# Kernel tuning notes

Hardware: AMD Instinct MI355X
Metric: run time of the kernel (lower is better)

## Reference

```python
import jax, jax.numpy as jnp
import numpy as np

P, N, H, W, K = 100000, 8, 256, 256, 8
EPS = 1e-12  # F.normalize clamp_min eps


def setup_inputs() -> dict:
    key = jax.random.key(0)
    ks = jax.random.split(key, 12)
    normals = jax.random.normal(ks[3], (P, 3), jnp.float32)
    normals = normals / jnp.linalg.norm(normals, axis=-1, keepdims=True)
    return {
        "idx": jax.random.randint(ks[0], (N, H, W, K), 0, P),
        "dists": jax.random.uniform(ks[1], (N, H, W, K), dtype=jnp.float32),
        "points": jax.random.normal(ks[2], (P, 3), jnp.float32),
        "normals": normals,
        "light_location": jax.random.normal(ks[4], (1, 3), jnp.float32) * 2.0,
        "light_ambient": jax.random.uniform(ks[5], (1, 3), dtype=jnp.float32),
        "light_diffuse": jax.random.uniform(ks[6], (1, 3), dtype=jnp.float32),
        "light_specular": jax.random.uniform(ks[7], (1, 3), dtype=jnp.float32),
        "mat_ambient": jax.random.uniform(ks[8], (1, 3), dtype=jnp.float32),
        "mat_diffuse": jax.random.uniform(ks[9], (1, 3), dtype=jnp.float32),
        "mat_specular": jax.random.uniform(ks[10], (1, 3), dtype=jnp.float32),
        "camera_position": jax.random.normal(ks[11], (1, 3), jnp.float32) * 3.0,
        "shininess": 64,
    }


def _normalize(v):
    return v / jnp.clip(jnp.linalg.norm(v, axis=-1, keepdims=True), 1e-6)


def reference(idx, dists, points, normals, light_location, light_ambient,
              light_diffuse, light_specular, mat_ambient, mat_diffuse,
              mat_specular, camera_position, shininess):
    # masked gather: invalid (idx < 0) pixels read point 0
    safe_idx = jnp.where(idx < 0, 0, idx)                      # (N,H,W,K)
    pix_pts = points[safe_idx]                                 # (N,H,W,K,3)
    pix_nrm = normals[safe_idx]                                # (N,H,W,K,3)

    # point-light Phong shading (pytorch3d _apply_lighting)
    dir_light = _normalize(light_location - pix_pts)           # (N,H,W,K,3)
    cos = jnp.sum(pix_nrm * dir_light, axis=-1, keepdims=True)  # (N,H,W,K,1)
    diffuse = light_diffuse * jax.nn.relu(cos) * mat_diffuse

    view = _normalize(camera_position - pix_pts)
    reflect = 2.0 * cos * pix_nrm - dir_light
    alpha = jax.nn.relu(jnp.sum(view * reflect, axis=-1)) * (cos[..., 0] > 0)
    specular = light_specular * (alpha ** shininess)[..., None] * mat_specular

    ambient = light_ambient * mat_ambient                      # (1,3) broadcast
    colors = ambient + diffuse + specular                      # (N,H,W,K,3)

    # L1-normalized distance weights over K, weighted sum
    dist_mask = jnp.where(dists != -1.0, dists, 0.0)
    wn = dist_mask / jnp.clip(jnp.sum(jnp.abs(dist_mask), axis=-1, keepdims=True), EPS)
    images = jnp.sum(wn[..., None] * colors, axis=-2)          # (N,H,W,3)
    return images
```

## Files before the change

### kernel.cpp

```cpp
#include <hip/hip_runtime.h>

#define K 8

typedef float vfloat4 __attribute__((ext_vector_type(4)));
typedef int   vint4   __attribute__((ext_vector_type(4)));

__global__ __launch_bounds__(256) void pack_pn_kernel(
    const float* __restrict__ points,
    const float* __restrict__ normals,
    vfloat4*     __restrict__ rec,
    int P)
{
    const int i = blockIdx.x * blockDim.x + threadIdx.x;
    if (i >= P) return;
    const size_t b = (size_t)i * 3;
    vfloat4 pv = {points[b],  points[b + 1],  points[b + 2],  0.0f};
    vfloat4 nv = {normals[b], normals[b + 1], normals[b + 2], 0.0f};
    rec[2 * i]     = pv;
    rec[2 * i + 1] = nv;
}

template <bool PACKED>
__global__ __launch_bounds__(256) void shading_compositor_kernel(
    const int*    __restrict__ idx,
    const float*  __restrict__ dists,
    const float*  __restrict__ points,
    const float*  __restrict__ normals,
    const vfloat4* __restrict__ rec,
    const float*  __restrict__ light_location,
    const float*  __restrict__ light_ambient,
    const float*  __restrict__ light_diffuse,
    const float*  __restrict__ light_specular,
    const float*  __restrict__ mat_ambient,
    const float*  __restrict__ mat_diffuse,
    const float*  __restrict__ mat_specular,
    const float*  __restrict__ camera_position,
    const int*    __restrict__ shininess_p,
    float*        __restrict__ out,
    int n_pix)
{
    const int p = blockIdx.x * blockDim.x + threadIdx.x;
    if (p >= n_pix) return;

    const vint4*   idxv = reinterpret_cast<const vint4*>(idx   + (size_t)p * K);
    const vfloat4* dstv = reinterpret_cast<const vfloat4*>(dists + (size_t)p * K);
    vint4   i0 = __builtin_nontemporal_load(idxv);
    vint4   i1 = __builtin_nontemporal_load(idxv + 1);
    vfloat4 d0 = __builtin_nontemporal_load(dstv);
    vfloat4 d1 = __builtin_nontemporal_load(dstv + 1);

    int   ik[K] = {i0.x, i0.y, i0.z, i0.w, i1.x, i1.y, i1.z, i1.w};
    float dk[K] = {d0.x, d0.y, d0.z, d0.w, d1.x, d1.y, d1.z, d1.w};

    vfloat4 pr[K], nr[K];
#pragma unroll
    for (int k = 0; k < K; ++k) {
        const int ii = (ik[k] < 0) ? 0 : ik[k];
        if (PACKED) {
            const vfloat4* r = rec + 2 * (size_t)ii;
            pr[k] = r[0];
            nr[k] = r[1];
        } else {
            const size_t base = (size_t)ii * 3;
            vfloat4 pv = {points[base], points[base + 1], points[base + 2], 0.0f};
            vfloat4 nv = {normals[base], normals[base + 1], normals[base + 2], 0.0f};
            pr[k] = pv;
            nr[k] = nv;
        }
    }
#if defined(__has_builtin)
#if __has_builtin(__builtin_amdgcn_sched_barrier)
    __builtin_amdgcn_sched_barrier(0);
#endif
#endif

    const float Lx = light_location[0], Ly = light_location[1], Lz = light_location[2];
    const float Cx = camera_position[0], Cy = camera_position[1], Cz = camera_position[2];
    const float amb0 = light_ambient[0] * mat_ambient[0];
    const float amb1 = light_ambient[1] * mat_ambient[1];
    const float amb2 = light_ambient[2] * mat_ambient[2];
    const float dif0 = light_diffuse[0] * mat_diffuse[0];
    const float dif1 = light_diffuse[1] * mat_diffuse[1];
    const float dif2 = light_diffuse[2] * mat_diffuse[2];
    const float spc0 = light_specular[0] * mat_specular[0];
    const float spc1 = light_specular[1] * mat_specular[1];
    const float spc2 = light_specular[2] * mat_specular[2];
    const int   shin = shininess_p[0];

    float w[K];
    float wsum = 0.f;
#pragma unroll
    for (int k = 0; k < K; ++k) {
        float d = dk[k];
        float m = (d != -1.0f) ? d : 0.0f;
        w[k] = m;
        wsum += fabsf(m);
    }
    const float winv = 1.0f / fmaxf(wsum, 1e-12f);

    float acc0 = 0.f, acc1 = 0.f, acc2 = 0.f;

#pragma unroll
    for (int k = 0; k < K; ++k) {
        const float px = pr[k].x, py = pr[k].y, pz = pr[k].z;
        const float nx = nr[k].x, ny = nr[k].y, nz = nr[k].z;

        float lx = Lx - px, ly = Ly - py, lz = Lz - pz;
        float ll = lx * lx + ly * ly + lz * lz;
        float li = (ll > 1e-12f) ? rsqrtf(ll) : 1e6f;
        lx *= li; ly *= li; lz *= li;

        const float cosv = nx * lx + ny * ly + nz * lz;

        float vx = Cx - px, vy = Cy - py, vz = Cz - pz;
        float vv = vx * vx + vy * vy + vz * vz;
        float vi = (vv > 1e-12f) ? rsqrtf(vv) : 1e6f;
        vx *= vi; vy *= vi; vz *= vi;

        const float c2 = 2.0f * cosv;
        const float rx = c2 * nx - lx;
        const float ry = c2 * ny - ly;
        const float rz = c2 * nz - lz;

        float alpha = fmaxf(vx * rx + vy * ry + vz * rz, 0.0f);
        if (!(cosv > 0.0f)) alpha = 0.0f;

        float sp;
        if (shin == 64) {
            float b = alpha;
            b *= b; b *= b; b *= b; b *= b; b *= b; b *= b;
            sp = b;
        } else {
            sp = 1.0f;
            float b = alpha;
            int e = shin;
            while (e > 0) {
                if (e & 1) sp *= b;
                b *= b;
                e >>= 1;
            }
        }

        const float rc = fmaxf(cosv, 0.0f);
        const float wk = w[k];
        acc0 += wk * (amb0 + dif0 * rc + spc0 * sp);
        acc1 += wk * (amb1 + dif1 * rc + spc1 * sp);
        acc2 += wk * (amb2 + dif2 * rc + spc2 * sp);
    }

    float* o = out + (size_t)p * 3;
    __builtin_nontemporal_store(acc0 * winv, o);
    __builtin_nontemporal_store(acc1 * winv, o + 1);
    __builtin_nontemporal_store(acc2 * winv, o + 2);
}

extern "C" void kernel_launch(void* const* d_in, const int* in_sizes, int n_in,
                              void* d_out, int out_size, void* d_ws, size_t ws_size,
                              hipStream_t stream) {
    const int*   idx             = (const int*)d_in[0];
    const float* dists           = (const float*)d_in[1];
    const float* points          = (const float*)d_in[2];
    const float* normals         = (const float*)d_in[3];
    const float* light_location  = (const float*)d_in[4];
    const float* light_ambient   = (const float*)d_in[5];
    const float* light_diffuse   = (const float*)d_in[6];
    const float* light_specular  = (const float*)d_in[7];
    const float* mat_ambient     = (const float*)d_in[8];
    const float* mat_diffuse     = (const float*)d_in[9];
    const float* mat_specular    = (const float*)d_in[10];
    const float* camera_position = (const float*)d_in[11];
    const int*   shininess       = (const int*)d_in[12];
    float*       out             = (float*)d_out;

    const int n_pix = in_sizes[0] / K;
    const int P     = in_sizes[2] / 3;

    const int block = 256;
    const int grid  = (n_pix + block - 1) / block;

    const size_t need = (size_t)P * 2 * sizeof(vfloat4);
    if (ws_size >= need) {
        vfloat4* rec = (vfloat4*)d_ws;
        pack_pn_kernel<<<(P + block - 1) / block, block, 0, stream>>>(points, normals, rec, P);
        shading_compositor_kernel<true><<<grid, block, 0, stream>>>(
            idx, dists, points, normals, rec, light_location, light_ambient,
            light_diffuse, light_specular, mat_ambient, mat_diffuse,
            mat_specular, camera_position, shininess, out, n_pix);
    } else {
        shading_compositor_kernel<false><<<grid, block, 0, stream>>>(
            idx, dists, points, normals, nullptr, light_location, light_ambient,
            light_diffuse, light_specular, mat_ambient, mat_diffuse,
            mat_specular, camera_position, shininess, out, n_pix);
    }
}
```

Before: 127.4 us.

## Pack normals as 16-bit octahedral into point record w channel

The pack kernel now encodes each unit normal as two 16-bit octahedral coordinates stored in the w lane of the point vector, so each point record shrinks from 32 bytes to 16 bytes. The shading kernel gathers one 16-byte record per sample and decodes the normal with a few ALU ops and an rsqrt. This halves the random-gather footprint and traffic, at the cost of quantization error in the normals, which the high specular exponent can amplify. The scheduling barrier after the gathers is also removed.

```diff
diff --git a/kernel.cpp b/kernel.cpp
--- a/kernel.cpp
+++ b/kernel.cpp
@@ -14,10 +14,21 @@
     const int i = blockIdx.x * blockDim.x + threadIdx.x;
     if (i >= P) return;
     const size_t b = (size_t)i * 3;
-    vfloat4 pv = {points[b],  points[b + 1],  points[b + 2],  0.0f};
-    vfloat4 nv = {normals[b], normals[b + 1], normals[b + 2], 0.0f};
-    rec[2 * i]     = pv;
-    rec[2 * i + 1] = nv;
+    const float nx = normals[b], ny = normals[b + 1], nz = normals[b + 2];
+
+    const float s  = 1.0f / (fabsf(nx) + fabsf(ny) + fabsf(nz));
+    float ox = nx * s, oy = ny * s;
+    if (nz < 0.0f) {
+        const float tx = (1.0f - fabsf(oy)) * (ox >= 0.0f ? 1.0f : -1.0f);
+        const float ty = (1.0f - fabsf(ox)) * (oy >= 0.0f ? 1.0f : -1.0f);
+        ox = tx; oy = ty;
+    }
+    const unsigned ux = (unsigned)(fminf(fmaxf(ox * 0.5f + 0.5f, 0.0f), 1.0f) * 65535.0f + 0.5f);
+    const unsigned uy = (unsigned)(fminf(fmaxf(oy * 0.5f + 0.5f, 0.0f), 1.0f) * 65535.0f + 0.5f);
+    const unsigned pk = ux | (uy << 16);
+
+    vfloat4 r = {points[b], points[b + 1], points[b + 2], __uint_as_float(pk)};
+    rec[i] = r;
 }
 
 template <bool PACKED>
@@ -52,27 +63,28 @@
     int   ik[K] = {i0.x, i0.y, i0.z, i0.w, i1.x, i1.y, i1.z, i1.w};
     float dk[K] = {d0.x, d0.y, d0.z, d0.w, d1.x, d1.y, d1.z, d1.w};
 
-    vfloat4 pr[K], nr[K];
+    vfloat4 rr[K];
 #pragma unroll
     for (int k = 0; k < K; ++k) {
         const int ii = (ik[k] < 0) ? 0 : ik[k];
         if (PACKED) {
-            const vfloat4* r = rec + 2 * (size_t)ii;
-            pr[k] = r[0];
-            nr[k] = r[1];
+            rr[k] = rec[(size_t)ii];
         } else {
             const size_t base = (size_t)ii * 3;
             vfloat4 pv = {points[base], points[base + 1], points[base + 2], 0.0f};
+            rr[k] = pv;
+        }
+    }
+    vfloat4 nrf[K];
+    if (!PACKED) {
+#pragma unroll
+        for (int k = 0; k < K; ++k) {
+            const int ii = (ik[k] < 0) ? 0 : ik[k];
+            const size_t base = (size_t)ii * 3;
             vfloat4 nv = {normals[base], normals[base + 1], normals[base + 2], 0.0f};
-            pr[k] = pv;
-            nr[k] = nv;
-        }
-    }
-#if defined(__has_builtin)
-#if __has_builtin(__builtin_amdgcn_sched_barrier)
-    __builtin_amdgcn_sched_barrier(0);
-#endif
-#endif
+            nrf[k] = nv;
+        }
+    }
 
     const float Lx = light_location[0], Ly = light_location[1], Lz = light_location[2];
     const float Cx = camera_position[0], Cy = camera_position[1], Cz = camera_position[2];
@@ -102,8 +114,22 @@
 
 #pragma unroll
     for (int k = 0; k < K; ++k) {
-        const float px = pr[k].x, py = pr[k].y, pz = pr[k].z;
-        const float nx = nr[k].x, ny = nr[k].y, nz = nr[k].z;
+        const float px = rr[k].x, py = rr[k].y, pz = rr[k].z;
+
+        float nx, ny, nz;
+        if (PACKED) {
+            const unsigned pk = __float_as_uint(rr[k].w);
+            const float ox = (float)(pk & 0xffffu) * (2.0f / 65535.0f) - 1.0f;
+            const float oy = (float)(pk >> 16)     * (2.0f / 65535.0f) - 1.0f;
+            float zz = 1.0f - fabsf(ox) - fabsf(oy);
+            const float t = fmaxf(-zz, 0.0f);
+            float xx = ox + ((ox >= 0.0f) ? -t : t);
+            float yy = oy + ((oy >= 0.0f) ? -t : t);
+            const float ni = rsqrtf(xx * xx + yy * yy + zz * zz);
+            nx = xx * ni; ny = yy * ni; nz = zz * ni;
+        } else {
+            nx = nrf[k].x; ny = nrf[k].y; nz = nrf[k].z;
+        }
 
         float lx = Lx - px, ly = Ly - py, lz = Lz - pz;
         float ll = lx * lx + ly * ly + lz * lz;
@@ -178,7 +204,7 @@
     const int block = 256;
     const int grid  = (n_pix + block - 1) / block;
 
-    const size_t need = (size_t)P * 2 * sizeof(vfloat4);
+    const size_t need = (size_t)P * sizeof(vfloat4);
     if (ws_size >= need) {
         vfloat4* rec = (vfloat4*)d_ws;
         pack_pn_kernel<<<(P + block - 1) / block, block, 0, stream>>>(points, normals, rec, P);
```

Result: no change. 125.0 us (-1.9%).

## Precompute per-point shaded colors into fp16 table and gather colors per pixel

Applied to the files above, without the earlier changes.

Moves the Phong lighting computation from per-pixel-sample to a per-point prepass that writes a compact fp16 RGB color table. The compositor then gathers 8-byte color entries and does only the weighted sum. This removes redundant lighting math for each of the K samples and shrinks random-gather traffic from two float4 records to one 8-byte record. It trades accuracy for this, since colors are rounded to half precision.

```diff
diff --git a/kernel.cpp b/kernel.cpp
--- a/kernel.cpp
+++ b/kernel.cpp
@@ -1,32 +1,91 @@
 #include <hip/hip_runtime.h>
+#include <hip/hip_fp16.h>
 
 #define K 8
 
-typedef float vfloat4 __attribute__((ext_vector_type(4)));
-typedef int   vint4   __attribute__((ext_vector_type(4)));
-
-__global__ __launch_bounds__(256) void pack_pn_kernel(
+typedef float    vfloat4 __attribute__((ext_vector_type(4)));
+typedef int      vint4   __attribute__((ext_vector_type(4)));
+typedef unsigned vuint2  __attribute__((ext_vector_type(2)));
+
+__global__ __launch_bounds__(256) void shade_points_kernel(
     const float* __restrict__ points,
     const float* __restrict__ normals,
-    vfloat4*     __restrict__ rec,
+    const float* __restrict__ light_location,
+    const float* __restrict__ light_ambient,
+    const float* __restrict__ light_diffuse,
+    const float* __restrict__ light_specular,
+    const float* __restrict__ mat_ambient,
+    const float* __restrict__ mat_diffuse,
+    const float* __restrict__ mat_specular,
+    const float* __restrict__ camera_position,
+    const int*   __restrict__ shininess_p,
+    vuint2*      __restrict__ ctab,
     int P)
 {
     const int i = blockIdx.x * blockDim.x + threadIdx.x;
     if (i >= P) return;
+
     const size_t b = (size_t)i * 3;
-    vfloat4 pv = {points[b],  points[b + 1],  points[b + 2],  0.0f};
-    vfloat4 nv = {normals[b], normals[b + 1], normals[b + 2], 0.0f};
-    rec[2 * i]     = pv;
-    rec[2 * i + 1] = nv;
+    const float px = points[b],  py = points[b + 1],  pz = points[b + 2];
+    const float nx = normals[b], ny = normals[b + 1], nz = normals[b + 2];
+
+    const float Lx = light_location[0], Ly = light_location[1], Lz = light_location[2];
+    const float Cx = camera_position[0], Cy = camera_position[1], Cz = camera_position[2];
+    const int   shin = shininess_p[0];
+
+    float lx = Lx - px, ly = Ly - py, lz = Lz - pz;
+    float ll = lx * lx + ly * ly + lz * lz;
+    float li = (ll > 1e-12f) ? rsqrtf(ll) : 1e6f;
+    lx *= li; ly *= li; lz *= li;
+
+    const float cosv = nx * lx + ny * ly + nz * lz;
+
+    float vx = Cx - px, vy = Cy - py, vz = Cz - pz;
+    float vv = vx * vx + vy * vy + vz * vz;
+    float vi = (vv > 1e-12f) ? rsqrtf(vv) : 1e6f;
+    vx *= vi; vy *= vi; vz *= vi;
+
+    const float c2 = 2.0f * cosv;
+    const float rx = c2 * nx - lx;
+    const float ry = c2 * ny - ly;
+    const float rz = c2 * nz - lz;
+
+    float alpha = fmaxf(vx * rx + vy * ry + vz * rz, 0.0f);
+    if (!(cosv > 0.0f)) alpha = 0.0f;
+
+    float sp = 1.0f, bb = alpha;
+    int e = shin;
+    while (e > 0) {
+        if (e & 1) sp *= bb;
+        bb *= bb;
+        e >>= 1;
+    }
+
+    const float rc = fmaxf(cosv, 0.0f);
+    const float c0 = light_ambient[0] * mat_ambient[0]
+                   + light_diffuse[0] * mat_diffuse[0] * rc
+                   + light_specular[0] * mat_specular[0] * sp;
+    const float c1 = light_ambient[1] * mat_ambient[1]
+                   + light_diffuse[1] * mat_diffuse[1] * rc
+                   + light_specular[1] * mat_specular[1] * sp;
+    const float c2c = light_ambient[2] * mat_ambient[2]
+                   + light_diffuse[2] * mat_diffuse[2] * rc
+                   + light_specular[2] * mat_specular[2] * sp;
+
+    const unsigned h0 = __half_as_ushort(__float2half(c0));
+    const unsigned h1 = __half_as_ushort(__float2half(c1));
+    const unsigned h2 = __half_as_ushort(__float2half(c2c));
+    vuint2 r = {h0 | (h1 << 16), h2};
+    ctab[i] = r;
 }
 
 template <bool PACKED>
-__global__ __launch_bounds__(256) void shading_compositor_kernel(
+__global__ __launch_bounds__(256) void composite_kernel(
     const int*    __restrict__ idx,
     const float*  __restrict__ dists,
+    const vuint2* __restrict__ ctab,
     const float*  __restrict__ points,
     const float*  __restrict__ normals,
-    const vfloat4* __restrict__ rec,
     const float*  __restrict__ light_location,
     const float*  __restrict__ light_ambient,
     const float*  __restrict__ light_diffuse,
@@ -52,40 +111,12 @@
     int   ik[K] = {i0.x, i0.y, i0.z, i0.w, i1.x, i1.y, i1.z, i1.w};
     float dk[K] = {d0.x, d0.y, d0.z, d0.w, d1.x, d1.y, d1.z, d1.w};
 
-    vfloat4 pr[K], nr[K];
+    vuint2 cv[K];
 #pragma unroll
     for (int k = 0; k < K; ++k) {
         const int ii = (ik[k] < 0) ? 0 : ik[k];
-        if (PACKED) {
-            const vfloat4* r = rec + 2 * (size_t)ii;
-            pr[k] = r[0];
-            nr[k] = r[1];
-        } else {
-            const size_t base = (size_t)ii * 3;
-            vfloat4 pv = {points[base], points[base + 1], points[base + 2], 0.0f};
-            vfloat4 nv = {normals[base], normals[base + 1], normals[base + 2], 0.0f};
-            pr[k] = pv;
-            nr[k] = nv;
-        }
-    }
-#if defined(__has_builtin)
-#if __has_builtin(__builtin_amdgcn_sched_barrier)
-    __builtin_amdgcn_sched_barrier(0);
-#endif
-#endif
-
-    const float Lx = light_location[0], Ly = light_location[1], Lz = light_location[2];
-    const float Cx = camera_position[0], Cy = camera_position[1], Cz = camera_position[2];
-    const float amb0 = light_ambient[0] * mat_ambient[0];
-    const float amb1 = light_ambient[1] * mat_ambient[1];
-    const float amb2 = light_ambient[2] * mat_ambient[2];
-    const float dif0 = light_diffuse[0] * mat_diffuse[0];
-    const float dif1 = light_diffuse[1] * mat_diffuse[1];
-    const float dif2 = light_diffuse[2] * mat_diffuse[2];
-    const float spc0 = light_specular[0] * mat_specular[0];
-    const float spc1 = light_specular[1] * mat_specular[1];
-    const float spc2 = light_specular[2] * mat_specular[2];
-    const int   shin = shininess_p[0];
+        if (PACKED) cv[k] = ctab[(size_t)ii];
+    }
 
     float w[K];
     float wsum = 0.f;
@@ -100,52 +131,66 @@
 
     float acc0 = 0.f, acc1 = 0.f, acc2 = 0.f;
 
-#pragma unroll
-    for (int k = 0; k < K; ++k) {
-        const float px = pr[k].x, py = pr[k].y, pz = pr[k].z;
-        const float nx = nr[k].x, ny = nr[k].y, nz = nr[k].z;
-
-        float lx = Lx - px, ly = Ly - py, lz = Lz - pz;
-        float ll = lx * lx + ly * ly + lz * lz;
-        float li = (ll > 1e-12f) ? rsqrtf(ll) : 1e6f;
-        lx *= li; ly *= li; lz *= li;
-
-        const float cosv = nx * lx + ny * ly + nz * lz;
-
-        float vx = Cx - px, vy = Cy - py, vz = Cz - pz;
-        float vv = vx * vx + vy * vy + vz * vz;
-        float vi = (vv > 1e-12f) ? rsqrtf(vv) : 1e6f;
-        vx *= vi; vy *= vi; vz *= vi;
-
-        const float c2 = 2.0f * cosv;
-        const float rx = c2 * nx - lx;
-        const float ry = c2 * ny - ly;
-        const float rz = c2 * nz - lz;
-
-        float alpha = fmaxf(vx * rx + vy * ry + vz * rz, 0.0f);
-        if (!(cosv > 0.0f)) alpha = 0.0f;
-
-        float sp;
-        if (shin == 64) {
-            float b = alpha;
-            b *= b; b *= b; b *= b; b *= b; b *= b; b *= b;
-            sp = b;
-        } else {
-            sp = 1.0f;
-            float b = alpha;
+    if (PACKED) {
+#pragma unroll
+        for (int k = 0; k < K; ++k) {
+            const float c0 = __half2float(__ushort_as_half((unsigned short)(cv[k].x & 0xffffu)));
+            const float c1 = __half2float(__ushort_as_half((unsigned short)(cv[k].x >> 16)));
+            const float c2 = __half2float(__ushort_as_half((unsigned short)(cv[k].y & 0xffffu)));
+            const float wk = w[k];
+            acc0 += wk * c0;
+            acc1 += wk * c1;
+            acc2 += wk * c2;
+        }
+    } else {
+        const float Lx = light_location[0], Ly = light_location[1], Lz = light_location[2];
+        const float Cx = camera_position[0], Cy = camera_position[1], Cz = camera_position[2];
+        const float amb0 = light_ambient[0] * mat_ambient[0];
+        const float amb1 = light_ambient[1] * mat_ambient[1];
+        const float amb2 = light_ambient[2] * mat_ambient[2];
+        const float dif0 = light_diffuse[0] * mat_diffuse[0];
+        const float dif1 = light_diffuse[1] * mat_diffuse[1];
+        const float dif2 = light_diffuse[2] * mat_diffuse[2];
+        const float spc0 = light_specular[0] * mat_specular[0];
+        const float spc1 = light_specular[1] * mat_specular[1];
+        const float spc2 = light_specular[2] * mat_specular[2];
+        const int   shin = shininess_p[0];
+#pragma unroll
+        for (int k = 0; k < K; ++k) {
+            const int ii = (ik[k] < 0) ? 0 : ik[k];
+            const size_t base = (size_t)ii * 3;
+            const float px = points[base], py = points[base + 1], pz = points[base + 2];
+            const float nx = normals[base], ny = normals[base + 1], nz = normals[base + 2];
+
+            float lx = Lx - px, ly = Ly - py, lz = Lz - pz;
+            float ll = lx * lx + ly * ly + lz * lz;
+            float li = (ll > 1e-12f) ? rsqrtf(ll) : 1e6f;
+            lx *= li; ly *= li; lz *= li;
+            const float cosv = nx * lx + ny * ly + nz * lz;
+
+            float vx = Cx - px, vy = Cy - py, vz = Cz - pz;
+            float vv = vx * vx + vy * vy + vz * vz;
+            float vi = (vv > 1e-12f) ? rsqrtf(vv) : 1e6f;
+            vx *= vi; vy *= vi; vz *= vi;
+
+            const float c2 = 2.0f * cosv;
+            const float rx = c2 * nx - lx;
+            const float ry = c2 * ny - ly;
+            const float rz = c2 * nz - lz;
+
+            float alpha = fmaxf(vx * rx + vy * ry + vz * rz, 0.0f);
+            if (!(cosv > 0.0f)) alpha = 0.0f;
+
+            float sp = 1.0f, bb = alpha;
             int e = shin;
-            while (e > 0) {
-                if (e & 1) sp *= b;
-                b *= b;
-                e >>= 1;
-            }
+            while (e > 0) { if (e & 1) sp *= bb; bb *= bb; e >>= 1; }
+
+            const float rc = fmaxf(cosv, 0.0f);
+            const float wk = w[k];
+            acc0 += wk * (amb0 + dif0 * rc + spc0 * sp);
+            acc1 += wk * (amb1 + dif1 * rc + spc1 * sp);
+            acc2 += wk * (amb2 + dif2 * rc + spc2 * sp);
         }
-
-        const float rc = fmaxf(cosv, 0.0f);
-        const float wk = w[k];
-        acc0 += wk * (amb0 + dif0 * rc + spc0 * sp);
-        acc1 += wk * (amb1 + dif1 * rc + spc1 * sp);
-        acc2 += wk * (amb2 + dif2 * rc + spc2 * sp);
     }
 
     float* o = out + (size_t)p * 3;
@@ -178,17 +223,20 @@
     const int block = 256;
     const int grid  = (n_pix + block - 1) / block;
 
-    const size_t need = (size_t)P * 2 * sizeof(vfloat4);
+    const size_t need = (size_t)P * sizeof(vuint2);
     if (ws_size >= need) {
-        vfloat4* rec = (vfloat4*)d_ws;
-        pack_pn_kernel<<<(P + block - 1) / block, block, 0, stream>>>(points, normals, rec, P);
-        shading_compositor_kernel<true><<<grid, block, 0, stream>>>(
-            idx, dists, points, normals, rec, light_location, light_ambient,
+        vuint2* ctab = (vuint2*)d_ws;
+        shade_points_kernel<<<(P + block - 1) / block, block, 0, stream>>>(
+            points, normals, light_location, light_ambient, light_diffuse,
+            light_specular, mat_ambient, mat_diffuse, mat_specular,
+            camera_position, shininess, ctab, P);
+        composite_kernel<true><<<grid, block, 0, stream>>>(
+            idx, dists, ctab, points, normals, light_location, light_ambient,
             light_diffuse, light_specular, mat_ambient, mat_diffuse,
             mat_specular, camera_position, shininess, out, n_pix);
     } else {
-        shading_compositor_kernel<false><<<grid, block, 0, stream>>>(
-            idx, dists, points, normals, nullptr, light_location, light_ambient,
+        composite_kernel<false><<<grid, block, 0, stream>>>(
+            idx, dists, nullptr, points, normals, light_location, light_ambient,
             light_diffuse, light_specular, mat_ambient, mat_diffuse,
             mat_specular, camera_position, shininess, out, n_pix);
     }
```

After: 126.6 us. About the same (-0.6%).
